# Kernel optimization log

Measured on AMD Instinct MI355X. Metric: run time of the kernel, lower is better.

Reference implementation:

```python
import jax, jax.numpy as jnp
import numpy as np

B, S, D_MODEL, D_FF, E, K = 4, 2048, 1024, 4096, 8, 2
CAP_FACTOR = 1.0


def setup_inputs() -> dict:
    key = jax.random.key(0)
    ks = jax.random.split(key, 6)
    std = 0.02
    return {
        "x": jax.random.normal(ks[0], (B, S, D_MODEL), jnp.float32),
        "router_w": jax.random.normal(ks[1], (E, D_MODEL), jnp.float32) * std,  # Linear(d_model,E,bias=False) weight
        "w1": jax.random.normal(ks[2], (E, D_MODEL, D_FF), jnp.float32) * std,
        "b1": jnp.zeros((E, D_FF), jnp.float32),
        "w2": jax.random.normal(ks[3], (E, D_FF, D_MODEL), jnp.float32) * std,
        "b2": jnp.zeros((E, D_MODEL), jnp.float32),
    }


def reference(x, router_w, w1, b1, w2, b2):
    b, s, d = x.shape
    T = b * s
    e = router_w.shape[0]
    capacity = int(CAP_FACTOR * T / e)  # static
    xf = x.reshape(T, d)

    # --- routing ---
    logits = xf @ router_w.T                       # [T,E]
    probs = jax.nn.softmax(logits, axis=-1)
    vals, idx = jax.lax.top_k(probs, K)            # [T,K] values / expert ids
    vals = vals / vals.sum(-1, keepdims=True)

    # dense gate matrix [T,E]; top_k experts are distinct so this is a scatter of K weights per token
    ar = jnp.arange(T)
    gates = jnp.zeros((T, e), x.dtype).at[ar[:, None], idx].add(vals)

    # --- load-balancing loss ---
    counts = jnp.zeros((e,), jnp.float32).at[idx.reshape(-1)].add(1.0)
    ideal = T * K / e
    lb_loss = jnp.sum((counts - ideal) ** 2) / (T ** 2)

    # --- capacity-limited dispatch (first `capacity` tokens in token order per expert) ---
    mask = gates > 0                                               # [T,E]
    order = jnp.argsort(jnp.logical_not(mask), axis=0)[:capacity]  # stable: assigned tokens first, ascending token id -> [cap,E]
    valid = jnp.take_along_axis(mask, order, axis=0)               # [cap,E] token actually assigned & within capacity
    idx_ec = order.T                                               # [E,cap]

    # --- grouped expert MLP ---
    xg = xf[idx_ec]                                                # [E,cap,D]
    h = jax.nn.gelu(jnp.einsum('ecd,edf->ecf', xg, w1) + b1[:, None, :], approximate=False)
    y = jnp.einsum('ecf,efd->ecd', h, w2) + b2[:, None, :]         # [E,cap,D]

    # --- combine (scatter-add with routing weights; dropped/invalid slots get weight 0) ---
    wt = gates[idx_ec, jnp.arange(e)[:, None]] * valid.T           # [E,cap]
    out = jnp.zeros((T, d), x.dtype).at[idx_ec.reshape(-1)].add((y * wt[..., None]).reshape(-1, d))
    return out.reshape(b, s, d), lb_loss
```

## Files before the change

### kernel.cpp

```cpp
#include <hip/hip_runtime.h>
#include <hip/hip_bf16.h>

#define T_TOK 8192
#define DMODEL 1024
#define DFF 4096
#define NEXP 8
#define CAP 1024

typedef __attribute__((ext_vector_type(8))) __bf16 bf16x8;
typedef __attribute__((ext_vector_type(4))) float f32x4;

__device__ __forceinline__ unsigned short f2bf(float f) {
  union { float f; unsigned int u; } v;
  v.f = f;
  return (unsigned short)((v.u + 0x7fffu + ((v.u >> 16) & 1u)) >> 16);
}

__device__ __forceinline__ float fast_gelu(float v) {
  float x = fabsf(v) * 0.70710678118654752440f;
  float t = __builtin_amdgcn_rcpf(1.0f + 0.3275911f * x);
  float poly = t * (0.254829592f + t * (-0.284496736f + t * (1.421413741f +
               t * (-1.453152027f + t * 1.061405429f))));
  float er = 1.0f - poly * __expf(-x * x);
  float s = (v >= 0.0f) ? er : -er;
  return 0.5f * v * (1.0f + s);
}

__device__ __forceinline__ void load_lds16(const unsigned short* g, unsigned short* l) {
  __builtin_amdgcn_global_load_lds((const __attribute__((address_space(1))) void*)g,
                                   (__attribute__((address_space(3))) void*)l,
                                   16, 0, 0);
}

__global__ void k_router(const float* __restrict__ x, const float* __restrict__ rw,
                         unsigned short* __restrict__ xb,
                         int* __restrict__ tk_idx, float* __restrict__ tk_w) {
  int wv = threadIdx.x >> 6, lane = threadIdx.x & 63;
  int t = blockIdx.x * 4 + wv;
  const float4* xr = (const float4*)(x + (size_t)t * DMODEL);
  uint2* xbw = (uint2*)(xb + (size_t)t * DMODEL);
  float acc[NEXP];
#pragma unroll
  for (int e = 0; e < NEXP; ++e) acc[e] = 0.f;
#pragma unroll
  for (int j = 0; j < DMODEL / 256; ++j) {
    float4 v = xr[j * 64 + lane];
#pragma unroll
    for (int e = 0; e < NEXP; ++e) {
      float4 w = ((const float4*)(rw + e * DMODEL))[j * 64 + lane];
      acc[e] += v.x * w.x + v.y * w.y + v.z * w.z + v.w * w.w;
    }
    uint2 p;
    p.x = (unsigned int)f2bf(v.x) | ((unsigned int)f2bf(v.y) << 16);
    p.y = (unsigned int)f2bf(v.z) | ((unsigned int)f2bf(v.w) << 16);
    xbw[j * 64 + lane] = p;
  }
#pragma unroll
  for (int e = 0; e < NEXP; ++e)
    for (int off = 32; off; off >>= 1) acc[e] += __shfl_xor(acc[e], off);
  if (lane == 0) {
    int i0 = 0;
    for (int e = 1; e < NEXP; ++e) if (acc[e] > acc[i0]) i0 = e;
    int i1 = (i0 == 0) ? 1 : 0;
    for (int e = 0; e < NEXP; ++e) if (e != i0 && acc[e] > acc[i1]) i1 = e;
    float ex = expf(acc[i1] - acc[i0]);
    float w0 = 1.f / (1.f + ex);
    float w1 = ex / (1.f + ex);
    tk_idx[2 * t] = i0; tk_idx[2 * t + 1] = i1;
    tk_w[2 * t] = w0;  tk_w[2 * t + 1] = w1;
  }
}

__global__ void k_transpose_cvt(const float* __restrict__ src, unsigned short* __restrict__ dst,
                                int Kd, int Nd) {
  __shared__ unsigned short tile[64][73];
  int e = blockIdx.z;
  size_t k0 = (size_t)blockIdx.y * 64, n0 = (size_t)blockIdx.x * 64;
  int tid = threadIdx.x;
  const float* sb = src + (size_t)e * Kd * Nd;
  int r = tid >> 4, cg = (tid & 15) * 4;
  for (int rr = 0; rr < 4; ++rr) {
    int row = r + rr * 16;
    float4 v = *(const float4*)(sb + (k0 + row) * Nd + n0 + cg);
    tile[row][cg + 0] = f2bf(v.x);
    tile[row][cg + 1] = f2bf(v.y);
    tile[row][cg + 2] = f2bf(v.z);
    tile[row][cg + 3] = f2bf(v.w);
  }
  __syncthreads();
  unsigned short* db = dst + (size_t)e * Nd * Kd;
  int rn = tid >> 3, kg = (tid & 7) * 8;
  for (int rr = 0; rr < 2; ++rr) {
    int nrow = rn + rr * 32;
    union { unsigned short h[8]; uint4 v; } o;
#pragma unroll
    for (int j = 0; j < 8; ++j) o.h[j] = tile[kg + j][nrow];
    *(uint4*)(db + (n0 + nrow) * Kd + k0 + kg) = o.v;
  }
}

__global__ void k_scan(const int* __restrict__ tk_idx, const float* __restrict__ tk_w,
                       int* __restrict__ etok, float* __restrict__ egate,
                       float* __restrict__ loss_out) {
  __shared__ int wavecnt[16][NEXP];
  __shared__ int waveoff[16][NEXP];
  __shared__ int offs[NEXP];
  __shared__ int ctot[NEXP];
  int tid = threadIdx.x;
  int lane = tid & 63, wv = tid >> 6;
  if (tid < NEXP) offs[tid] = 0;
  for (int i = tid; i < NEXP * CAP; i += 1024) { etok[i] = 0; egate[i] = 0.f; }
  __syncthreads();
  unsigned long long lt = (1ULL << lane) - 1ULL;
  for (int c = 0; c < T_TOK / 1024; ++c) {
    int t = c * 1024 + tid;
    int e0 = tk_idx[2 * t], e1 = tk_idx[2 * t + 1];
    float w0 = tk_w[2 * t], w1 = tk_w[2 * t + 1];
    int p0 = 0, p1 = 0;
#pragma unroll
    for (int e = 0; e < NEXP; ++e) {
      unsigned long long bal = __ballot((e0 == e) || (e1 == e));
      if (e0 == e) p0 = __popcll(bal & lt);
      if (e1 == e) p1 = __popcll(bal & lt);
      if (lane == 0) wavecnt[wv][e] = __popcll(bal);
    }
    __syncthreads();
    if (tid < NEXP) {
      int s = 0;
      for (int w = 0; w < 16; ++w) { waveoff[w][tid] = s; s += wavecnt[w][tid]; }
      ctot[tid] = s;
    }
    __syncthreads();
    int r0 = offs[e0] + waveoff[wv][e0] + p0;
    int r1 = offs[e1] + waveoff[wv][e1] + p1;
    if (r0 < CAP) { etok[e0 * CAP + r0] = t; egate[e0 * CAP + r0] = w0; }
    if (r1 < CAP) { etok[e1 * CAP + r1] = t; egate[e1 * CAP + r1] = w1; }
    __syncthreads();
    if (tid < NEXP) offs[tid] += ctot[tid];
    __syncthreads();
  }
  if (tid == 0) {
    float loss = 0.f;
    for (int e = 0; e < NEXP; ++e) {
      float d = (float)offs[e] - 2048.0f;
      loss += d * d;
    }
    loss_out[0] = loss / (8192.0f * 8192.0f);
  }
}

__global__ __launch_bounds__(256) void k_gemm1(
    const unsigned short* __restrict__ xb, const unsigned short* __restrict__ w1t,
    const float* __restrict__ b1, const int* __restrict__ etok,
    unsigned short* __restrict__ H) {
  __shared__ unsigned short smem[4 * 64 * 72];
  unsigned short* As = smem;
  unsigned short* Bs = smem + 4096;
  int tid = threadIdx.x;
  int lane = tid & 63, wv = tid >> 6;
  int bid = blockIdx.x;
  int e = bid >> 8;
  int b = bid & 255;
  int nl = b & 7, m = (b >> 3) & 7, nh = b >> 6;
  int m0 = m * 128, n0 = (nh * 8 + nl) * 128;

  const unsigned short* gA[2];
  const unsigned short* gB[2];
  unsigned short* lA[2];
  unsigned short* lB[2];
#pragma unroll
  for (int s = 0; s < 2; ++s) {
    int i = s * 256 + tid;
    int row = i >> 2, cb = (i & 3) * 8;
    int tok = etok[e * CAP + m0 + row];
    gA[s] = xb + (size_t)tok * DMODEL + cb;
    gB[s] = w1t + ((size_t)e * DFF + n0 + row) * DMODEL + cb;
    int wb = (s * 256 + wv * 64) * 8;
    lA[s] = As + wb;
    lB[s] = Bs + wb;
  }

  f32x4 zero = {0.f, 0.f, 0.f, 0.f};
  f32x4 acc[4][4];
#pragma unroll
  for (int mi = 0; mi < 4; ++mi)
#pragma unroll
    for (int ni = 0; ni < 4; ++ni) acc[mi][ni] = zero;

  int wm = (wv >> 1) * 64, wn = (wv & 1) * 64;
  int fr = lane & 15, quad = lane >> 4;
  const unsigned short* pa = As + (wm + fr) * 32 + quad * 8;
  const unsigned short* pb = Bs + (wn + fr) * 32 + quad * 8;

  for (int k0 = 0; k0 < DMODEL; k0 += 32) {
#pragma unroll
    for (int s = 0; s < 2; ++s) {
      load_lds16(gA[s] + k0, lA[s]);
      load_lds16(gB[s] + k0, lB[s]);
    }
    __syncthreads();
    bf16x8 av[4], bv[4];
#pragma unroll
    for (int mi = 0; mi < 4; ++mi) av[mi] = *(const bf16x8*)(pa + mi * 16 * 32);
#pragma unroll
    for (int ni = 0; ni < 4; ++ni) bv[ni] = *(const bf16x8*)(pb + ni * 16 * 32);
#pragma unroll
    for (int mi = 0; mi < 4; ++mi)
#pragma unroll
      for (int ni = 0; ni < 4; ++ni)
        acc[mi][ni] = __builtin_amdgcn_mfma_f32_16x16x32_bf16(bv[ni], av[mi], acc[mi][ni], 0, 0, 0);
    __syncthreads();
  }

  unsigned short* L = smem + wv * (64 * 72);
#pragma unroll
  for (int ni = 0; ni < 4; ++ni) {
    float4 b4 = *(const float4*)(b1 + e * DFF + n0 + wn + ni * 16 + quad * 4);
#pragma unroll
    for (int mi = 0; mi < 4; ++mi) {
      float v0 = fast_gelu(acc[mi][ni][0] + b4.x);
      float v1 = fast_gelu(acc[mi][ni][1] + b4.y);
      float v2 = fast_gelu(acc[mi][ni][2] + b4.z);
      float v3 = fast_gelu(acc[mi][ni][3] + b4.w);
      uint2 p;
      p.x = (unsigned int)f2bf(v0) | ((unsigned int)f2bf(v1) << 16);
      p.y = (unsigned int)f2bf(v2) | ((unsigned int)f2bf(v3) << 16);
      *(uint2*)(L + (mi * 16 + fr) * 72 + ni * 16 + quad * 4) = p;
    }
  }
  int crow = lane >> 3, cchunk = lane & 7;
#pragma unroll
  for (int t = 0; t < 8; ++t) {
    int row = t * 8 + crow;
    uint4 v = *(const uint4*)(L + row * 72 + cchunk * 8);
    *(uint4*)(H + ((size_t)e * CAP + m0 + wm + row) * DFF + n0 + wn + cchunk * 8) = v;
  }
}

__global__ __launch_bounds__(256) void k_gemm2(
    const unsigned short* __restrict__ H, const unsigned short* __restrict__ w2t,
    const float* __restrict__ b2, const int* __restrict__ etok,
    const float* __restrict__ egate, float* __restrict__ out) {
  __shared__ unsigned short As[128 * 32];
  __shared__ unsigned short Bs[128 * 32];
  int tid = threadIdx.x;
  int lane = tid & 63, wv = tid >> 6;
  int bid = blockIdx.x;
  int e = bid >> 6;
  int b = bid & 63;
  int m0 = (b >> 3) * 128, n0 = (b & 7) * 128;

  const unsigned short* gA[2];
  const unsigned short* gB[2];
  unsigned short* lA[2];
  unsigned short* lB[2];
#pragma unroll
  for (int s = 0; s < 2; ++s) {
    int i = s * 256 + tid;
    int row = i >> 2, cb = (i & 3) * 8;
    gA[s] = H + ((size_t)e * CAP + m0 + row) * DFF + cb;
    gB[s] = w2t + ((size_t)e * DMODEL + n0 + row) * DFF + cb;
    int wb = (s * 256 + wv * 64) * 8;
    lA[s] = As + wb;
    lB[s] = Bs + wb;
  }

  f32x4 zero = {0.f, 0.f, 0.f, 0.f};
  f32x4 acc[4][4];
#pragma unroll
  for (int mi = 0; mi < 4; ++mi)
#pragma unroll
    for (int ni = 0; ni < 4; ++ni) acc[mi][ni] = zero;

  int wm = (wv >> 1) * 64, wn = (wv & 1) * 64;
  int fr = lane & 15, quad = lane >> 4;
  const unsigned short* pa = As + (wm + fr) * 32 + quad * 8;
  const unsigned short* pb = Bs + (wn + fr) * 32 + quad * 8;

  for (int k0 = 0; k0 < DFF; k0 += 32) {
#pragma unroll
    for (int s = 0; s < 2; ++s) {
      load_lds16(gA[s] + k0, lA[s]);
      load_lds16(gB[s] + k0, lB[s]);
    }
    __syncthreads();
    bf16x8 av[4], bv[4];
#pragma unroll
    for (int mi = 0; mi < 4; ++mi) av[mi] = *(const bf16x8*)(pa + mi * 16 * 32);
#pragma unroll
    for (int ni = 0; ni < 4; ++ni) bv[ni] = *(const bf16x8*)(pb + ni * 16 * 32);
#pragma unroll
    for (int mi = 0; mi < 4; ++mi)
#pragma unroll
      for (int ni = 0; ni < 4; ++ni)
        acc[mi][ni] = __builtin_amdgcn_mfma_f32_16x16x32_bf16(av[mi], bv[ni], acc[mi][ni], 0, 0, 0);
    __syncthreads();
  }

  float bs[4];
  int cols[4];
#pragma unroll
  for (int ni = 0; ni < 4; ++ni) {
    cols[ni] = n0 + wn + ni * 16 + fr;
    bs[ni] = b2[e * DMODEL + cols[ni]];
  }
#pragma unroll
  for (int mi = 0; mi < 4; ++mi) {
    int mbase = m0 + wm + mi * 16 + quad * 4;
#pragma unroll
    for (int rr = 0; rr < 4; ++rr) {
      int mrow = mbase + rr;
      int tok = etok[e * CAP + mrow];
      float g = egate[e * CAP + mrow];
      if (g != 0.f) {
        float* orow = out + (size_t)tok * DMODEL;
#pragma unroll
        for (int ni = 0; ni < 4; ++ni)
          atomicAdd(orow + cols[ni], g * (acc[mi][ni][rr] + bs[ni]));
      }
    }
  }
}

extern "C" void kernel_launch(void* const* d_in, const int* in_sizes, int n_in,
                              void* d_out, int out_size, void* d_ws, size_t ws_size,
                              hipStream_t stream) {
  (void)in_sizes; (void)n_in; (void)ws_size;
  const float* x  = (const float*)d_in[0];
  const float* rw = (const float*)d_in[1];
  const float* w1 = (const float*)d_in[2];
  const float* b1 = (const float*)d_in[3];
  const float* w2 = (const float*)d_in[4];
  const float* b2 = (const float*)d_in[5];
  float* out = (float*)d_out;

  char* ws = (char*)d_ws;
  const size_t XB_BYTES = (size_t)T_TOK * DMODEL * 2;
  const size_t WT_BYTES = (size_t)NEXP * DFF * DMODEL * 2;
  const size_t H_BYTES  = (size_t)NEXP * CAP * DFF * 2;
  unsigned short* xb = (unsigned short*)ws;
  unsigned short* wT = (unsigned short*)(ws + XB_BYTES);
  unsigned short* Hb = (unsigned short*)(ws + XB_BYTES + WT_BYTES);
  char* small = ws + XB_BYTES + WT_BYTES + H_BYTES;
  int*   etok  = (int*)small;
  float* egate = (float*)(small + NEXP * CAP * 4);
  int*   tkidx = (int*)(small + 2 * NEXP * CAP * 4);
  float* tkw   = (float*)(small + 2 * NEXP * CAP * 4 + T_TOK * 2 * 4);

  hipMemsetAsync(d_out, 0, (size_t)out_size * sizeof(float), stream);
  k_router<<<T_TOK / 4, 256, 0, stream>>>(x, rw, xb, tkidx, tkw);
  k_scan<<<1, 1024, 0, stream>>>(tkidx, tkw, etok, egate,
                                 (float*)d_out + (size_t)T_TOK * DMODEL);
  k_transpose_cvt<<<dim3(DFF / 64, DMODEL / 64, NEXP), 256, 0, stream>>>(w1, wT, DMODEL, DFF);
  k_gemm1<<<NEXP * 256, 256, 0, stream>>>(xb, wT, b1, etok, Hb);
  k_transpose_cvt<<<dim3(DMODEL / 64, DFF / 64, NEXP), 256, 0, stream>>>(w2, wT, DFF, DMODEL);
  k_gemm2<<<NEXP * 64, 256, 0, stream>>>(Hb, wT, b2, etok, egate, out);
}
```

Before: 579.1 us.

## Split GEMM2 K dimension in two and shrink GEMM1 epilogue LDS staging

GEMM2 now launches twice as many blocks, each reducing over half of the D_FF dimension, and combines the two partial results through the existing atomicAdd combine. Only the first half adds the bias. The goal is to fill more CUs, since the old grid of 512 blocks underfilled the GPU. GEMM1's epilogue now stages each 16-column slice through a smaller per-wave LDS buffer, which cuts shared memory per block and may allow higher occupancy. The cost is twice as many atomic adds on the output and somewhat narrower global stores in GEMM1.

```diff
diff --git a/kernel.cpp b/kernel.cpp
--- a/kernel.cpp
+++ b/kernel.cpp
@@ -153,7 +153,7 @@
     const unsigned short* __restrict__ xb, const unsigned short* __restrict__ w1t,
     const float* __restrict__ b1, const int* __restrict__ etok,
     unsigned short* __restrict__ H) {
-  __shared__ unsigned short smem[4 * 64 * 72];
+  __shared__ __align__(16) unsigned short smem[8192];
   unsigned short* As = smem;
   unsigned short* Bs = smem + 4096;
   int tid = threadIdx.x;
@@ -212,7 +212,7 @@
     __syncthreads();
   }
 
-  unsigned short* L = smem + wv * (64 * 72);
+  unsigned short* EP = smem + wv * 1536;
 #pragma unroll
   for (int ni = 0; ni < 4; ++ni) {
     float4 b4 = *(const float4*)(b1 + e * DFF + n0 + wn + ni * 16 + quad * 4);
@@ -225,15 +225,14 @@
       uint2 p;
       p.x = (unsigned int)f2bf(v0) | ((unsigned int)f2bf(v1) << 16);
       p.y = (unsigned int)f2bf(v2) | ((unsigned int)f2bf(v3) << 16);
-      *(uint2*)(L + (mi * 16 + fr) * 72 + ni * 16 + quad * 4) = p;
-    }
-  }
-  int crow = lane >> 3, cchunk = lane & 7;
-#pragma unroll
-  for (int t = 0; t < 8; ++t) {
-    int row = t * 8 + crow;
-    uint4 v = *(const uint4*)(L + row * 72 + cchunk * 8);
-    *(uint4*)(H + ((size_t)e * CAP + m0 + wm + row) * DFF + n0 + wn + cchunk * 8) = v;
+      *(uint2*)(EP + (mi * 16 + fr) * 24 + quad * 4) = p;
+    }
+#pragma unroll
+    for (int t = 0; t < 2; ++t) {
+      int row = t * 32 + (lane >> 1), chunk = lane & 1;
+      uint4 v = *(const uint4*)(EP + row * 24 + chunk * 8);
+      *(uint4*)(H + ((size_t)e * CAP + m0 + wm + row) * DFF + n0 + wn + ni * 16 + chunk * 8) = v;
+    }
   }
 }
 
@@ -241,14 +240,17 @@
     const unsigned short* __restrict__ H, const unsigned short* __restrict__ w2t,
     const float* __restrict__ b2, const int* __restrict__ etok,
     const float* __restrict__ egate, float* __restrict__ out) {
-  __shared__ unsigned short As[128 * 32];
-  __shared__ unsigned short Bs[128 * 32];
+  __shared__ __align__(16) unsigned short smem[8192];
+  unsigned short* As = smem;
+  unsigned short* Bs = smem + 4096;
   int tid = threadIdx.x;
   int lane = tid & 63, wv = tid >> 6;
   int bid = blockIdx.x;
-  int e = bid >> 6;
-  int b = bid & 63;
-  int m0 = (b >> 3) * 128, n0 = (b & 7) * 128;
+  int e = bid >> 7;
+  int ks = (bid >> 6) & 1;
+  int m0 = ((bid >> 3) & 7) * 128;
+  int n0 = (bid & 7) * 128;
+  int kbase = ks * (DFF / 2);
 
   const unsigned short* gA[2];
   const unsigned short* gB[2];
@@ -258,8 +260,8 @@
   for (int s = 0; s < 2; ++s) {
     int i = s * 256 + tid;
     int row = i >> 2, cb = (i & 3) * 8;
-    gA[s] = H + ((size_t)e * CAP + m0 + row) * DFF + cb;
-    gB[s] = w2t + ((size_t)e * DMODEL + n0 + row) * DFF + cb;
+    gA[s] = H + ((size_t)e * CAP + m0 + row) * DFF + kbase + cb;
+    gB[s] = w2t + ((size_t)e * DMODEL + n0 + row) * DFF + kbase + cb;
     int wb = (s * 256 + wv * 64) * 8;
     lA[s] = As + wb;
     lB[s] = Bs + wb;
@@ -277,7 +279,7 @@
   const unsigned short* pa = As + (wm + fr) * 32 + quad * 8;
   const unsigned short* pb = Bs + (wn + fr) * 32 + quad * 8;
 
-  for (int k0 = 0; k0 < DFF; k0 += 32) {
+  for (int k0 = 0; k0 < DFF / 2; k0 += 32) {
 #pragma unroll
     for (int s = 0; s < 2; ++s) {
       load_lds16(gA[s] + k0, lA[s]);
@@ -302,7 +304,7 @@
 #pragma unroll
   for (int ni = 0; ni < 4; ++ni) {
     cols[ni] = n0 + wn + ni * 16 + fr;
-    bs[ni] = b2[e * DMODEL + cols[ni]];
+    bs[ni] = (ks == 0) ? b2[e * DMODEL + cols[ni]] : 0.0f;
   }
 #pragma unroll
   for (int mi = 0; mi < 4; ++mi) {
@@ -354,5 +356,5 @@
   k_transpose_cvt<<<dim3(DFF / 64, DMODEL / 64, NEXP), 256, 0, stream>>>(w1, wT, DMODEL, DFF);
   k_gemm1<<<NEXP * 256, 256, 0, stream>>>(xb, wT, b1, etok, Hb);
   k_transpose_cvt<<<dim3(DMODEL / 64, DFF / 64, NEXP), 256, 0, stream>>>(w2, wT, DFF, DMODEL);
-  k_gemm2<<<NEXP * 64, 256, 0, stream>>>(Hb, wT, b2, etok, egate, out);
-}
+  k_gemm2<<<NEXP * 128, 256, 0, stream>>>(Hb, wT, b2, etok, egate, out);
+}
```

Result: slower. 610.4 us (+5.4%).
